# Performance work log

Measured on AMD Instinct MI355X. Metric: run time of the kernel, lower is better.

The kernel has to match this reference:

```python
import jax, jax.numpy as jnp
import numpy as np

D = 1024
K = 256
B = 8192


def setup_inputs() -> dict:
    key = jax.random.key(0)
    kx, kw, kd, kp = jax.random.split(key, 4)
    x = jax.random.normal(kx, (B, D), dtype=jnp.float32)
    # scale weights ~1/sqrt(d) so the 11-matmul chain stays numerically sane
    Ws = jax.random.normal(kw, (10, D, D), dtype=jnp.float32) / jnp.sqrt(jnp.float32(D))
    W_dec = jax.random.normal(kd, (D, K), dtype=jnp.float32) / jnp.sqrt(jnp.float32(K))
    perm = jax.random.randint(kp, (K,), 0, D, dtype=jnp.int64)
    return {"x": x, "Ws": Ws, "W_dec": W_dec, "perm": perm}


def reference(x, Ws, W_dec, perm):
    # torch nn.Linear(d,d,bias=False): y = x @ W.T
    # source applies fc1..fc9, then fc9 AGAIN, then fc10 (11 matmuls, 10 weights)
    order = list(range(9)) + [8, 9]
    h = x
    for i in order:
        h = h @ Ws[i].T  # [B, D]
    y = h[:, perm]        # vectorized gather, replaces per-row python loop [B, K]
    out = y @ W_dec.T     # fc_decode: [B, D]
    return out
```

## Files before the change

### kernel.cpp

```cpp
#include <hip/hip_runtime.h>
#include <stdint.h>
#include <stddef.h>

typedef __bf16 bf16;
typedef __bf16 bf16x8 __attribute__((ext_vector_type(8)));
typedef float f32x4 __attribute__((ext_vector_type(4)));

__device__ __forceinline__ void global_to_lds16(const void* g, void* l) {
  const __attribute__((address_space(1))) unsigned* gp =
      reinterpret_cast<const __attribute__((address_space(1))) unsigned*>(
          reinterpret_cast<uintptr_t>(g));
  __attribute__((address_space(3))) unsigned* lp =
      reinterpret_cast<__attribute__((address_space(3))) unsigned*>(
          reinterpret_cast<uintptr_t>(l));
  __builtin_amdgcn_global_load_lds(gp, lp, 16, 0, 0);
}

__device__ __forceinline__ void tile8x8_swizzle(int t, int& bx, int& by) {
  bx = (((t >> 3) & 1) << 2) | (t & 3);
  by = (((t >> 4) & 3) << 1) | ((t >> 2) & 1);
}

template <typename OutT>
__device__ __forceinline__ void gemm128_body(const bf16* __restrict__ A,
                                             const bf16* __restrict__ B,
                                             OutT* __restrict__ C,
                                             int bx, int by) {
  __shared__ bf16 As[2][128 * 64];
  __shared__ bf16 Bs[2][128 * 64];

  const int tid = threadIdx.x;
  const int wave = tid >> 6, lane = tid & 63;
  const int quad = lane >> 4, l16 = lane & 15;
  const int rowBase = by * 128;
  const int colBase = bx * 128;
  const int waveM = (wave >> 1) * 64, waveN = (wave & 1) * 64;

  const int sr = tid >> 2;
  const int sc = (tid & 3) * 8;
  const bf16* Ag0 = A + (size_t)(rowBase + sr) * 1024 + sc;
  const bf16* Ag1 = Ag0 + (size_t)64 * 1024;
  const bf16* Bg0 = B + (size_t)(colBase + sr) * 1024 + sc;
  const bf16* Bg1 = Bg0 + (size_t)64 * 1024;

  const int woff = wave * 1024;

  auto issue = [&](int k0, int p) {
    char* aB = (char*)As[p] + woff;
    char* bB = (char*)Bs[p] + woff;
    global_to_lds16(Ag0 + k0,      aB);
    global_to_lds16(Ag1 + k0,      aB + 4096);
    global_to_lds16(Ag0 + k0 + 32, aB + 8192);
    global_to_lds16(Ag1 + k0 + 32, aB + 12288);
    global_to_lds16(Bg0 + k0,      bB);
    global_to_lds16(Bg1 + k0,      bB + 4096);
    global_to_lds16(Bg0 + k0 + 32, bB + 8192);
    global_to_lds16(Bg1 + k0 + 32, bB + 12288);
  };

  f32x4 acc[4][4] = {};

  issue(0, 0);
  int p = 0;
#pragma unroll 1
  for (int k0 = 0; k0 < 1024; k0 += 64, p ^= 1) {
    __syncthreads();
    if (k0 + 64 < 1024) issue(k0 + 64, p ^ 1);
#pragma unroll
    for (int kk = 0; kk < 2; kk++) {
      const bf16* base = As[p] + kk * 4096;
      const bf16* baseB = Bs[p] + kk * 4096;
      bf16x8 af[4], bfr[4];
#pragma unroll
      for (int mi = 0; mi < 4; mi++)
        af[mi] = *(const bf16x8*)(base + (waveM + mi * 16 + l16) * 32 + quad * 8);
#pragma unroll
      for (int ni = 0; ni < 4; ni++)
        bfr[ni] = *(const bf16x8*)(baseB + (waveN + ni * 16 + l16) * 32 + quad * 8);
#pragma unroll
      for (int mi = 0; mi < 4; mi++)
#pragma unroll
        for (int ni = 0; ni < 4; ni++)
          acc[mi][ni] = __builtin_amdgcn_mfma_f32_16x16x32_bf16(af[mi], bfr[ni],
                                                                acc[mi][ni], 0, 0, 0);
    }
  }

  OutT* Cb = C + (size_t)(rowBase + waveM) * 1024 + colBase + waveN;
#pragma unroll
  for (int mi = 0; mi < 4; mi++)
#pragma unroll
    for (int ni = 0; ni < 4; ni++)
#pragma unroll
      for (int r = 0; r < 4; r++)
        Cb[(size_t)(mi * 16 + quad * 4 + r) * 1024 + ni * 16 + l16] =
            (OutT)acc[mi][ni][r];
}

struct PrepArgs {
  const float* cvt_src[5]; bf16* cvt_dst[5];
  const float* tr_src[6];  bf16* tr_dst[6];
  const float* Wdec; const int* praw; bf16* Gbf;
};

__global__ __launch_bounds__(256) void prep_all(PrepArgs p) {
  __shared__ alignas(16) char smem[64 * 65 * 2];
  const int b = blockIdx.x;
  const int tid = threadIdx.x;

  if (b < 2560) {
    const int m = b >> 9, blk = b & 511;
    const float* __restrict__ src = p.cvt_src[m];
    bf16* __restrict__ dst = p.cvt_dst[m];
    const int i = (blk * 256 + tid) * 8;
    float4 a = *(const float4*)(src + i);
    float4 c = *(const float4*)(src + i + 4);
    bf16x8 o;
    o[0] = (bf16)a.x; o[1] = (bf16)a.y; o[2] = (bf16)a.z; o[3] = (bf16)a.w;
    o[4] = (bf16)c.x; o[5] = (bf16)c.y; o[6] = (bf16)c.z; o[7] = (bf16)c.w;
    *(bf16x8*)(dst + i) = o;
  } else if (b < 4096) {
    const int t = b - 2560;
    const int m = t >> 8, r = t & 255;
    const float* __restrict__ src = p.tr_src[m];
    bf16* __restrict__ dst = p.tr_dst[m];
    bf16(*tile)[65] = reinterpret_cast<bf16(*)[65]>(smem);
    const int bx = (r & 15) * 64;
    const int by = (r >> 4) * 64;
    const int tx = tid & 63;
    const int ty4 = tid >> 6;
#pragma unroll
    for (int rr = 0; rr < 16; rr++) {
      int row = ty4 * 16 + rr;
      tile[row][tx] = (bf16)src[(size_t)(by + row) * 1024 + bx + tx];
    }
    __syncthreads();
#pragma unroll
    for (int rr = 0; rr < 16; rr++) {
      int row = ty4 * 16 + rr;
      dst[(size_t)(bx + row) * 1024 + by + tx] = tile[tx][row];
    }
  } else {
    const int j = b - 4096;
    float* row = (float*)smem;
    int* perm_l = (int*)(smem + 4096);
    int* nzp = (int*)(smem + 4096 + 1024);
#pragma unroll
    for (int c = 0; c < 4; c++) row[tid * 4 + c] = 0.f;
    if (tid == 0) *nzp = 0;
    __syncthreads();
    if (tid < 128 && p.praw[2 * tid + 1] != 0) atomicOr(nzp, 1);
    __syncthreads();
    const int is64 = (*nzp == 0);
    perm_l[tid] = is64 ? p.praw[2 * tid] : p.praw[tid];
    __syncthreads();
    atomicAdd(&row[perm_l[tid]], p.Wdec[(size_t)j * 256 + tid]);
    __syncthreads();
#pragma unroll
    for (int c = 0; c < 4; c++)
      p.Gbf[(size_t)j * 1024 + tid * 4 + c] = (bf16)row[tid * 4 + c];
  }
}

struct TreeArgs {
  const bf16* A[6]; const bf16* B[6]; bf16* C[6];
  int nG;
  const float* x; bf16* xbf; int ubase;
};

__global__ __launch_bounds__(256) void tree_level(TreeArgs a) {
  const int b = blockIdx.x;
  const int gBlocks = a.nG * 64;
  if (b < gBlocks) {
    const int z = b >> 6, t = b & 63;
    int bx, by;
    tile8x8_swizzle(t, bx, by);
    gemm128_body<bf16>(a.A[z], a.B[z], a.C[z], bx, by);
  } else {
    const int unit = a.ubase + (b - gBlocks);
    const int i = unit * 2048 + (int)threadIdx.x * 8;
    float4 v0 = *(const float4*)(a.x + i);
    float4 v1 = *(const float4*)(a.x + i + 4);
    bf16x8 o;
    o[0] = (bf16)v0.x; o[1] = (bf16)v0.y; o[2] = (bf16)v0.z; o[3] = (bf16)v0.w;
    o[4] = (bf16)v1.x; o[5] = (bf16)v1.y; o[6] = (bf16)v1.z; o[7] = (bf16)v1.w;
    *(bf16x8*)(a.xbf + i) = o;
  }
}

__global__ __launch_bounds__(256) void final_gemm(const bf16* __restrict__ A,
                                                  const bf16* __restrict__ B,
                                                  float* __restrict__ C) {
  const int b = blockIdx.x;
  gemm128_body<float>(A, B, C, b >> 6, b & 63);
}

extern "C" void kernel_launch(void* const* d_in, const int* in_sizes, int n_in,
                              void* d_out, int out_size, void* d_ws, size_t ws_size,
                              hipStream_t stream) {
  const float* x    = (const float*)d_in[0];
  const float* Wsrc = (const float*)d_in[1];
  const float* Wdec = (const float*)d_in[2];
  const int*   praw = (const int*)d_in[3];
  float* out = (float*)d_out;

  constexpr size_t MAT  = 1024ull * 1024ull;
  constexpr size_t SLOT = 2ull * 1024 * 1024;

  char* ws = (char*)d_ws;
  bf16* Wrm[5];
  for (int i = 0; i < 5; i++) Wrm[i] = (bf16*)(ws + (size_t)i * SLOT);
  bf16* Wt[6];
  for (int i = 0; i < 6; i++) Wt[i] = (bf16*)(ws + (size_t)(5 + i) * SLOT);
  bf16* Gbf = (bf16*)(ws + 11 * SLOT);
  bf16* xbf = (bf16*)(ws + 12 * SLOT);
  bf16* P[6];
  for (int i = 0; i < 6; i++) P[i] = (bf16*)(ws + (size_t)(20 + i) * SLOT);
  bf16* Q[3];
  for (int i = 0; i < 3; i++) Q[i] = (bf16*)(ws + (size_t)(26 + i) * SLOT);
  bf16* Rb = (bf16*)(ws + 29 * SLOT);
  bf16* Fb = (bf16*)(ws + 30 * SLOT);

  PrepArgs pa;
  const int rmIdx[5] = {1, 3, 5, 7, 8};
  for (int i = 0; i < 5; i++) { pa.cvt_src[i] = Wsrc + (size_t)rmIdx[i] * MAT; pa.cvt_dst[i] = Wrm[i]; }
  const int trIdx[6] = {0, 2, 4, 6, 8, 9};
  for (int i = 0; i < 6; i++) { pa.tr_src[i] = Wsrc + (size_t)trIdx[i] * MAT; pa.tr_dst[i] = Wt[i]; }
  pa.Wdec = Wdec; pa.praw = praw; pa.Gbf = Gbf;
  prep_all<<<dim3(5120), 256, 0, stream>>>(pa);

  TreeArgs L1{};
  const bf16* l1a[6] = {Gbf, Wt[4], Wrm[3], Wt[2], Wrm[1], Wt[0]};
  const bf16* l1b[6] = {Wt[5], Wrm[4], Wt[3], Wrm[2], Wt[1], Wrm[0]};
  for (int i = 0; i < 6; i++) { L1.A[i] = l1a[i]; L1.B[i] = l1b[i]; L1.C[i] = P[i]; }
  L1.nG = 6; L1.x = x; L1.xbf = xbf; L1.ubase = 0;
  tree_level<<<dim3(384), 256, 0, stream>>>(L1);

  TreeArgs L2{};
  const bf16* l2a[3] = {P[0], P[3], P[5]};
  const bf16* l2b[3] = {P[1], P[2], P[4]};
  for (int i = 0; i < 3; i++) { L2.A[i] = l2a[i]; L2.B[i] = l2b[i]; L2.C[i] = Q[i]; }
  L2.nG = 3; L2.x = x; L2.xbf = xbf; L2.ubase = 0;
  tree_level<<<dim3(192 + 1360), 256, 0, stream>>>(L2);

  TreeArgs L3{};
  L3.A[0] = Q[0]; L3.B[0] = Q[1]; L3.C[0] = Rb;
  L3.nG = 1; L3.x = x; L3.xbf = xbf; L3.ubase = 1360;
  tree_level<<<dim3(64 + 1360), 256, 0, stream>>>(L3);

  TreeArgs L4{};
  L4.A[0] = Rb; L4.B[0] = Q[2]; L4.C[0] = Fb;
  L4.nG = 1; L4.x = x; L4.xbf = xbf; L4.ubase = 2720;
  tree_level<<<dim3(64 + 1376), 256, 0, stream>>>(L4);

  final_gemm<<<dim3(512), 256, 0, stream>>>(xbf, Fb, out);

  (void)in_sizes; (void)n_in; (void)out_size; (void)ws_size;
}
```

Measured before the change: 197.1 us.

## Restructure matrix-chain tree to merge levels and overlap x-GEMM with weight products

Reassociates the weight-product tree so the activation GEMM (xbf times Q2) runs concurrently with the final weight-weight product (Q0·Q1) in one launch, removing one dependent level and kernel launch. The x-to-bf16 conversion now does eight units per block and is spread across the first two levels instead of three. This shortens the critical path of serial launches, but the final GEMM becomes S·R with both operands bf16 intermediates, which shifts where rounding happens. The changed pairing in L2 also alters the association order.

```diff
diff --git a/kernel.cpp b/kernel.cpp
--- a/kernel.cpp
+++ b/kernel.cpp
@@ -177,14 +177,34 @@
     tile8x8_swizzle(t, bx, by);
     gemm128_body<bf16>(a.A[z], a.B[z], a.C[z], bx, by);
   } else {
-    const int unit = a.ubase + (b - gBlocks);
-    const int i = unit * 2048 + (int)threadIdx.x * 8;
-    float4 v0 = *(const float4*)(a.x + i);
-    float4 v1 = *(const float4*)(a.x + i + 4);
-    bf16x8 o;
-    o[0] = (bf16)v0.x; o[1] = (bf16)v0.y; o[2] = (bf16)v0.z; o[3] = (bf16)v0.w;
-    o[4] = (bf16)v1.x; o[5] = (bf16)v1.y; o[6] = (bf16)v1.z; o[7] = (bf16)v1.w;
-    *(bf16x8*)(a.xbf + i) = o;
+    const int u0 = a.ubase + (b - gBlocks) * 8;
+#pragma unroll
+    for (int u = 0; u < 8; u++) {
+      const int i = (u0 + u) * 2048 + (int)threadIdx.x * 8;
+      float4 v0 = *(const float4*)(a.x + i);
+      float4 v1 = *(const float4*)(a.x + i + 4);
+      bf16x8 o;
+      o[0] = (bf16)v0.x; o[1] = (bf16)v0.y; o[2] = (bf16)v0.z; o[3] = (bf16)v0.w;
+      o[4] = (bf16)v1.x; o[5] = (bf16)v1.y; o[6] = (bf16)v1.z; o[7] = (bf16)v1.w;
+      *(bf16x8*)(a.xbf + i) = o;
+    }
+  }
+}
+
+struct L3SArgs {
+  const bf16* Q0; const bf16* Q1t; bf16* R;
+  const bf16* xbf; const bf16* Q2; bf16* S;
+};
+
+__global__ __launch_bounds__(256) void l3s_level(L3SArgs a) {
+  const int b = blockIdx.x;
+  if (b < 64) {
+    int bx, by;
+    tile8x8_swizzle(b, bx, by);
+    gemm128_body<bf16>(a.Q0, a.Q1t, a.R, bx, by);
+  } else {
+    const int t = b - 64;
+    gemm128_body<bf16>(a.xbf, a.Q2, a.S, t >> 6, t & 63);
   }
 }
 
@@ -219,7 +239,7 @@
   bf16* Q[3];
   for (int i = 0; i < 3; i++) Q[i] = (bf16*)(ws + (size_t)(26 + i) * SLOT);
   bf16* Rb = (bf16*)(ws + 29 * SLOT);
-  bf16* Fb = (bf16*)(ws + 30 * SLOT);
+  bf16* Sb = (bf16*)(ws + 31 * SLOT);
 
   PrepArgs pa;
   const int rmIdx[5] = {1, 3, 5, 7, 8};
@@ -234,26 +254,21 @@
   const bf16* l1b[6] = {Wt[5], Wrm[4], Wt[3], Wrm[2], Wt[1], Wrm[0]};
   for (int i = 0; i < 6; i++) { L1.A[i] = l1a[i]; L1.B[i] = l1b[i]; L1.C[i] = P[i]; }
   L1.nG = 6; L1.x = x; L1.xbf = xbf; L1.ubase = 0;
-  tree_level<<<dim3(384), 256, 0, stream>>>(L1);
+  tree_level<<<dim3(384 + 256), 256, 0, stream>>>(L1);
 
   TreeArgs L2{};
-  const bf16* l2a[3] = {P[0], P[3], P[5]};
-  const bf16* l2b[3] = {P[1], P[2], P[4]};
+  const bf16* l2a[3] = {P[0], P[3], P[4]};
+  const bf16* l2b[3] = {P[1], P[2], P[5]};
   for (int i = 0; i < 3; i++) { L2.A[i] = l2a[i]; L2.B[i] = l2b[i]; L2.C[i] = Q[i]; }
-  L2.nG = 3; L2.x = x; L2.xbf = xbf; L2.ubase = 0;
-  tree_level<<<dim3(192 + 1360), 256, 0, stream>>>(L2);
-
-  TreeArgs L3{};
-  L3.A[0] = Q[0]; L3.B[0] = Q[1]; L3.C[0] = Rb;
-  L3.nG = 1; L3.x = x; L3.xbf = xbf; L3.ubase = 1360;
-  tree_level<<<dim3(64 + 1360), 256, 0, stream>>>(L3);
-
-  TreeArgs L4{};
-  L4.A[0] = Rb; L4.B[0] = Q[2]; L4.C[0] = Fb;
-  L4.nG = 1; L4.x = x; L4.xbf = xbf; L4.ubase = 2720;
-  tree_level<<<dim3(64 + 1376), 256, 0, stream>>>(L4);
-
-  final_gemm<<<dim3(512), 256, 0, stream>>>(xbf, Fb, out);
+  L2.nG = 3; L2.x = x; L2.xbf = xbf; L2.ubase = 2048;
+  tree_level<<<dim3(192 + 256), 256, 0, stream>>>(L2);
+
+  L3SArgs l3;
+  l3.Q0 = Q[0]; l3.Q1t = Q[1]; l3.R = Rb;
+  l3.xbf = xbf; l3.Q2 = Q[2]; l3.S = Sb;
+  l3s_level<<<dim3(576), 256, 0, stream>>>(l3);
+
+  final_gemm<<<dim3(512), 256, 0, stream>>>(Sb, Rb, out);
 
   (void)in_sizes; (void)n_in; (void)out_size; (void)ws_size;
 }
```

Measured after the change: 201.7 us. 1.02x slower.

## Deepen GEMM LDS pipeline to four K=32 stages and rebalance x conversion blocks

Applied to the files above, without the earlier changes.

The 128x128 GEMM main loop now uses four K=32 LDS stages with three tiles in flight. It replaces __syncthreads with explicit vmcnt waits and a raw barrier, so global-to-LDS loads overlap more MFMA work. The x fp32-to-bf16 conversion blocks each handle eight units and are spread across levels 1 and 2 only, which shrinks the extra grids attached to levels 2 to 4. The manual waitcnt logic depends on exact instruction counts and adds race risk. It also changes how the conversion traffic overlaps with the GEMMs.

```diff
diff --git a/kernel.cpp b/kernel.cpp
--- a/kernel.cpp
+++ b/kernel.cpp
@@ -26,8 +26,8 @@
                                              const bf16* __restrict__ B,
                                              OutT* __restrict__ C,
                                              int bx, int by) {
-  __shared__ bf16 As[2][128 * 64];
-  __shared__ bf16 Bs[2][128 * 64];
+  __shared__ bf16 As[4][128 * 32];
+  __shared__ bf16 Bs[4][128 * 32];
 
   const int tid = threadIdx.x;
   const int wave = tid >> 6, lane = tid & 63;
@@ -45,45 +45,43 @@
 
   const int woff = wave * 1024;
 
-  auto issue = [&](int k0, int p) {
-    char* aB = (char*)As[p] + woff;
-    char* bB = (char*)Bs[p] + woff;
-    global_to_lds16(Ag0 + k0,      aB);
-    global_to_lds16(Ag1 + k0,      aB + 4096);
-    global_to_lds16(Ag0 + k0 + 32, aB + 8192);
-    global_to_lds16(Ag1 + k0 + 32, aB + 12288);
-    global_to_lds16(Bg0 + k0,      bB);
-    global_to_lds16(Bg1 + k0,      bB + 4096);
-    global_to_lds16(Bg0 + k0 + 32, bB + 8192);
-    global_to_lds16(Bg1 + k0 + 32, bB + 12288);
+  auto issue = [&](int k0, int c) {
+    char* aB = (char*)As[c] + woff;
+    char* bB = (char*)Bs[c] + woff;
+    global_to_lds16(Ag0 + k0, aB);
+    global_to_lds16(Ag1 + k0, aB + 4096);
+    global_to_lds16(Bg0 + k0, bB);
+    global_to_lds16(Bg1 + k0, bB + 4096);
   };
 
   f32x4 acc[4][4] = {};
 
-  issue(0, 0);
-  int p = 0;
+  issue(0, 0); issue(32, 1); issue(64, 2);
+
 #pragma unroll 1
-  for (int k0 = 0; k0 < 1024; k0 += 64, p ^= 1) {
-    __syncthreads();
-    if (k0 + 64 < 1024) issue(k0 + 64, p ^ 1);
-#pragma unroll
-    for (int kk = 0; kk < 2; kk++) {
-      const bf16* base = As[p] + kk * 4096;
-      const bf16* baseB = Bs[p] + kk * 4096;
-      bf16x8 af[4], bfr[4];
-#pragma unroll
-      for (int mi = 0; mi < 4; mi++)
-        af[mi] = *(const bf16x8*)(base + (waveM + mi * 16 + l16) * 32 + quad * 8);
+  for (int i = 0; i < 32; ++i) {
+    if (i < 30)       asm volatile("s_waitcnt vmcnt(8)" ::: "memory");
+    else if (i == 30) asm volatile("s_waitcnt vmcnt(4)" ::: "memory");
+    else              asm volatile("s_waitcnt vmcnt(0)" ::: "memory");
+    __builtin_amdgcn_s_barrier();
+    __builtin_amdgcn_sched_barrier(0);
+    if (i < 29) issue((i + 3) * 32, (i + 3) & 3);
+
+    const bf16* base  = As[i & 3];
+    const bf16* baseB = Bs[i & 3];
+    bf16x8 af[4], bfr[4];
+#pragma unroll
+    for (int mi = 0; mi < 4; mi++)
+      af[mi] = *(const bf16x8*)(base + (waveM + mi * 16 + l16) * 32 + quad * 8);
+#pragma unroll
+    for (int ni = 0; ni < 4; ni++)
+      bfr[ni] = *(const bf16x8*)(baseB + (waveN + ni * 16 + l16) * 32 + quad * 8);
+#pragma unroll
+    for (int mi = 0; mi < 4; mi++)
 #pragma unroll
       for (int ni = 0; ni < 4; ni++)
-        bfr[ni] = *(const bf16x8*)(baseB + (waveN + ni * 16 + l16) * 32 + quad * 8);
-#pragma unroll
-      for (int mi = 0; mi < 4; mi++)
-#pragma unroll
-        for (int ni = 0; ni < 4; ni++)
-          acc[mi][ni] = __builtin_amdgcn_mfma_f32_16x16x32_bf16(af[mi], bfr[ni],
-                                                                acc[mi][ni], 0, 0, 0);
-    }
+        acc[mi][ni] = __builtin_amdgcn_mfma_f32_16x16x32_bf16(af[mi], bfr[ni],
+                                                              acc[mi][ni], 0, 0, 0);
   }
 
   OutT* Cb = C + (size_t)(rowBase + waveM) * 1024 + colBase + waveN;
@@ -177,14 +175,17 @@
     tile8x8_swizzle(t, bx, by);
     gemm128_body<bf16>(a.A[z], a.B[z], a.C[z], bx, by);
   } else {
-    const int unit = a.ubase + (b - gBlocks);
-    const int i = unit * 2048 + (int)threadIdx.x * 8;
-    float4 v0 = *(const float4*)(a.x + i);
-    float4 v1 = *(const float4*)(a.x + i + 4);
-    bf16x8 o;
-    o[0] = (bf16)v0.x; o[1] = (bf16)v0.y; o[2] = (bf16)v0.z; o[3] = (bf16)v0.w;
-    o[4] = (bf16)v1.x; o[5] = (bf16)v1.y; o[6] = (bf16)v1.z; o[7] = (bf16)v1.w;
-    *(bf16x8*)(a.xbf + i) = o;
+    const int u0 = a.ubase + (b - gBlocks) * 8;
+#pragma unroll
+    for (int u = 0; u < 8; u++) {
+      const int i = (u0 + u) * 2048 + (int)threadIdx.x * 8;
+      float4 v0 = *(const float4*)(a.x + i);
+      float4 v1 = *(const float4*)(a.x + i + 4);
+      bf16x8 o;
+      o[0] = (bf16)v0.x; o[1] = (bf16)v0.y; o[2] = (bf16)v0.z; o[3] = (bf16)v0.w;
+      o[4] = (bf16)v1.x; o[5] = (bf16)v1.y; o[6] = (bf16)v1.z; o[7] = (bf16)v1.w;
+      *(bf16x8*)(a.xbf + i) = o;
+    }
   }
 }
 
@@ -234,24 +235,24 @@
   const bf16* l1b[6] = {Wt[5], Wrm[4], Wt[3], Wrm[2], Wt[1], Wrm[0]};
   for (int i = 0; i < 6; i++) { L1.A[i] = l1a[i]; L1.B[i] = l1b[i]; L1.C[i] = P[i]; }
   L1.nG = 6; L1.x = x; L1.xbf = xbf; L1.ubase = 0;
-  tree_level<<<dim3(384), 256, 0, stream>>>(L1);
+  tree_level<<<dim3(384 + 256), 256, 0, stream>>>(L1);
 
   TreeArgs L2{};
   const bf16* l2a[3] = {P[0], P[3], P[5]};
   const bf16* l2b[3] = {P[1], P[2], P[4]};
   for (int i = 0; i < 3; i++) { L2.A[i] = l2a[i]; L2.B[i] = l2b[i]; L2.C[i] = Q[i]; }
-  L2.nG = 3; L2.x = x; L2.xbf = xbf; L2.ubase = 0;
-  tree_level<<<dim3(192 + 1360), 256, 0, stream>>>(L2);
+  L2.nG = 3; L2.x = x; L2.xbf = xbf; L2.ubase = 2048;
+  tree_level<<<dim3(192 + 256), 256, 0, stream>>>(L2);
 
   TreeArgs L3{};
   L3.A[0] = Q[0]; L3.B[0] = Q[1]; L3.C[0] = Rb;
-  L3.nG = 1; L3.x = x; L3.xbf = xbf; L3.ubase = 1360;
-  tree_level<<<dim3(64 + 1360), 256, 0, stream>>>(L3);
+  L3.nG = 1; L3.x = x; L3.xbf = xbf; L3.ubase = 4096;
+  tree_level<<<dim3(64), 256, 0, stream>>>(L3);
 
   TreeArgs L4{};
   L4.A[0] = Rb; L4.B[0] = Q[2]; L4.C[0] = Fb;
-  L4.nG = 1; L4.x = x; L4.xbf = xbf; L4.ubase = 2720;
-  tree_level<<<dim3(64 + 1376), 256, 0, stream>>>(L4);
+  L4.nG = 1; L4.x = x; L4.xbf = xbf; L4.ubase = 4096;
+  tree_level<<<dim3(64), 256, 0, stream>>>(L4);
 
   final_gemm<<<dim3(512), 256, 0, stream>>>(xbf, Fb, out);
 
```

Result: slower. 209.6 us (+6.4%).

## Switch GEMMs to 256x128 tiles with 512 threads and XOR-swizzled LDS

Applied to the files above, without the earlier changes.

Replaces the 128x128 GEMM body with a 256x128 tile run by 8 waves. Staging now loads full 64-wide K rows with an XOR swizzle on the 16-byte chunk index, so fragment reads avoid LDS bank conflicts. The fp32-to-bf16 conversion of x moves into the first two tree levels, with 16 units per block, and the last two levels become pure GEMMs. The larger tile raises data reuse per block, but it halves the block count: the single-GEMM levels get only 32 blocks, and each block holds 96KB of LDS, which limits occupancy.

```diff
diff --git a/kernel.cpp b/kernel.cpp
--- a/kernel.cpp
+++ b/kernel.cpp
@@ -4,6 +4,7 @@
 
 typedef __bf16 bf16;
 typedef __bf16 bf16x8 __attribute__((ext_vector_type(8)));
+typedef __bf16 bf16x4 __attribute__((ext_vector_type(4)));
 typedef float f32x4 __attribute__((ext_vector_type(4)));
 
 __device__ __forceinline__ void global_to_lds16(const void* g, void* l) {
@@ -16,67 +17,63 @@
   __builtin_amdgcn_global_load_lds(gp, lp, 16, 0, 0);
 }
 
-__device__ __forceinline__ void tile8x8_swizzle(int t, int& bx, int& by) {
-  bx = (((t >> 3) & 1) << 2) | (t & 3);
-  by = (((t >> 4) & 3) << 1) | ((t >> 2) & 1);
-}
-
 template <typename OutT>
-__device__ __forceinline__ void gemm128_body(const bf16* __restrict__ A,
-                                             const bf16* __restrict__ B,
-                                             OutT* __restrict__ C,
-                                             int bx, int by) {
-  __shared__ bf16 As[2][128 * 64];
+__device__ __forceinline__ void gemm256x128_body(const bf16* __restrict__ A,
+                                                 const bf16* __restrict__ B,
+                                                 OutT* __restrict__ C,
+                                                 int bx, int by) {
+  __shared__ bf16 As[2][256 * 64];
   __shared__ bf16 Bs[2][128 * 64];
 
   const int tid = threadIdx.x;
   const int wave = tid >> 6, lane = tid & 63;
   const int quad = lane >> 4, l16 = lane & 15;
-  const int rowBase = by * 128;
+  const int rowBase = by * 256;
   const int colBase = bx * 128;
-  const int waveM = (wave >> 1) * 64, waveN = (wave & 1) * 64;
-
-  const int sr = tid >> 2;
-  const int sc = (tid & 3) * 8;
-  const bf16* Ag0 = A + (size_t)(rowBase + sr) * 1024 + sc;
-  const bf16* Ag1 = Ag0 + (size_t)64 * 1024;
-  const bf16* Bg0 = B + (size_t)(colBase + sr) * 1024 + sc;
-  const bf16* Bg1 = Bg0 + (size_t)64 * 1024;
-
-  const int woff = wave * 1024;
+  const int waveM = (wave >> 1) * 64;
+  const int waveN = (wave & 1) * 64;
+
+  const int srow = tid >> 3;
+  const int scol = (((tid & 7) ^ ((tid >> 3) & 7)) << 3);
+  const bf16* Ag = A + (size_t)(rowBase + srow) * 1024 + scol;
+  const bf16* Bg = B + (size_t)(colBase + srow) * 1024 + scol;
+  const int ldsoff = wave * 1024;
 
   auto issue = [&](int k0, int p) {
-    char* aB = (char*)As[p] + woff;
-    char* bB = (char*)Bs[p] + woff;
-    global_to_lds16(Ag0 + k0,      aB);
-    global_to_lds16(Ag1 + k0,      aB + 4096);
-    global_to_lds16(Ag0 + k0 + 32, aB + 8192);
-    global_to_lds16(Ag1 + k0 + 32, aB + 12288);
-    global_to_lds16(Bg0 + k0,      bB);
-    global_to_lds16(Bg1 + k0,      bB + 4096);
-    global_to_lds16(Bg0 + k0 + 32, bB + 8192);
-    global_to_lds16(Bg1 + k0 + 32, bB + 12288);
+    char* aB = (char*)As[p] + ldsoff;
+    char* bB = (char*)Bs[p] + ldsoff;
+#pragma unroll
+    for (int c = 0; c < 4; c++)
+      global_to_lds16(Ag + k0 + (size_t)c * 64 * 1024, aB + c * 8192);
+#pragma unroll
+    for (int c = 0; c < 2; c++)
+      global_to_lds16(Bg + k0 + (size_t)c * 64 * 1024, bB + c * 8192);
   };
 
   f32x4 acc[4][4] = {};
 
   issue(0, 0);
   int p = 0;
+  const int swz = l16 & 7;
 #pragma unroll 1
   for (int k0 = 0; k0 < 1024; k0 += 64, p ^= 1) {
     __syncthreads();
     if (k0 + 64 < 1024) issue(k0 + 64, p ^ 1);
 #pragma unroll
     for (int kk = 0; kk < 2; kk++) {
-      const bf16* base = As[p] + kk * 4096;
-      const bf16* baseB = Bs[p] + kk * 4096;
       bf16x8 af[4], bfr[4];
 #pragma unroll
-      for (int mi = 0; mi < 4; mi++)
-        af[mi] = *(const bf16x8*)(base + (waveM + mi * 16 + l16) * 32 + quad * 8);
-#pragma unroll
-      for (int ni = 0; ni < 4; ni++)
-        bfr[ni] = *(const bf16x8*)(baseB + (waveN + ni * 16 + l16) * 32 + quad * 8);
+      for (int mi = 0; mi < 4; mi++) {
+        const int row = waveM + mi * 16 + l16;
+        const int g = ((kk << 2) + quad) ^ swz;
+        af[mi] = *(const bf16x8*)(As[p] + row * 64 + g * 8);
+      }
+#pragma unroll
+      for (int ni = 0; ni < 4; ni++) {
+        const int row = waveN + ni * 16 + l16;
+        const int g = ((kk << 2) + quad) ^ swz;
+        bfr[ni] = *(const bf16x8*)(Bs[p] + row * 64 + g * 8);
+      }
 #pragma unroll
       for (int mi = 0; mi < 4; mi++)
 #pragma unroll
@@ -168,31 +165,33 @@
   const float* x; bf16* xbf; int ubase;
 };
 
-__global__ __launch_bounds__(256) void tree_level(TreeArgs a) {
+__global__ __launch_bounds__(512) void tree_level(TreeArgs a) {
   const int b = blockIdx.x;
-  const int gBlocks = a.nG * 64;
+  const int gBlocks = a.nG * 32;
   if (b < gBlocks) {
-    const int z = b >> 6, t = b & 63;
-    int bx, by;
-    tile8x8_swizzle(t, bx, by);
-    gemm128_body<bf16>(a.A[z], a.B[z], a.C[z], bx, by);
+    const int z = b >> 5, t = b & 31;
+    gemm256x128_body<bf16>(a.A[z], a.B[z], a.C[z], t >> 2, t & 3);
   } else {
-    const int unit = a.ubase + (b - gBlocks);
-    const int i = unit * 2048 + (int)threadIdx.x * 8;
-    float4 v0 = *(const float4*)(a.x + i);
-    float4 v1 = *(const float4*)(a.x + i + 4);
-    bf16x8 o;
-    o[0] = (bf16)v0.x; o[1] = (bf16)v0.y; o[2] = (bf16)v0.z; o[3] = (bf16)v0.w;
-    o[4] = (bf16)v1.x; o[5] = (bf16)v1.y; o[6] = (bf16)v1.z; o[7] = (bf16)v1.w;
-    *(bf16x8*)(a.xbf + i) = o;
+    const int u0 = a.ubase + (b - gBlocks) * 16;
+#pragma unroll
+    for (int u = 0; u < 16; u++) {
+      const int i = (u0 + u) * 2048 + (int)threadIdx.x * 4;
+      float4 v = *(const float4*)(a.x + i);
+      bf16x4 o;
+      o[0] = (bf16)v.x; o[1] = (bf16)v.y; o[2] = (bf16)v.z; o[3] = (bf16)v.w;
+      *(bf16x4*)(a.xbf + i) = o;
+    }
   }
 }
 
-__global__ __launch_bounds__(256) void final_gemm(const bf16* __restrict__ A,
+__global__ __launch_bounds__(512) void final_gemm(const bf16* __restrict__ A,
                                                   const bf16* __restrict__ B,
                                                   float* __restrict__ C) {
   const int b = blockIdx.x;
-  gemm128_body<float>(A, B, C, b >> 6, b & 63);
+  const int j = b >> 3;
+  const int by = (b & 7) * 4 + (j & 3);
+  const int bx = j >> 2;
+  gemm256x128_body<float>(A, B, C, bx, by);
 }
 
 extern "C" void kernel_launch(void* const* d_in, const int* in_sizes, int n_in,
@@ -234,26 +233,26 @@
   const bf16* l1b[6] = {Wt[5], Wrm[4], Wt[3], Wrm[2], Wt[1], Wrm[0]};
   for (int i = 0; i < 6; i++) { L1.A[i] = l1a[i]; L1.B[i] = l1b[i]; L1.C[i] = P[i]; }
   L1.nG = 6; L1.x = x; L1.xbf = xbf; L1.ubase = 0;
-  tree_level<<<dim3(384), 256, 0, stream>>>(L1);
+  tree_level<<<dim3(192 + 128), 512, 0, stream>>>(L1);
 
   TreeArgs L2{};
   const bf16* l2a[3] = {P[0], P[3], P[5]};
   const bf16* l2b[3] = {P[1], P[2], P[4]};
   for (int i = 0; i < 3; i++) { L2.A[i] = l2a[i]; L2.B[i] = l2b[i]; L2.C[i] = Q[i]; }
-  L2.nG = 3; L2.x = x; L2.xbf = xbf; L2.ubase = 0;
-  tree_level<<<dim3(192 + 1360), 256, 0, stream>>>(L2);
+  L2.nG = 3; L2.x = x; L2.xbf = xbf; L2.ubase = 2048;
+  tree_level<<<dim3(96 + 128), 512, 0, stream>>>(L2);
 
   TreeArgs L3{};
   L3.A[0] = Q[0]; L3.B[0] = Q[1]; L3.C[0] = Rb;
-  L3.nG = 1; L3.x = x; L3.xbf = xbf; L3.ubase = 1360;
-  tree_level<<<dim3(64 + 1360), 256, 0, stream>>>(L3);
+  L3.nG = 1; L3.x = x; L3.xbf = xbf; L3.ubase = 4096;
+  tree_level<<<dim3(32), 512, 0, stream>>>(L3);
 
   TreeArgs L4{};
   L4.A[0] = Rb; L4.B[0] = Q[2]; L4.C[0] = Fb;
-  L4.nG = 1; L4.x = x; L4.xbf = xbf; L4.ubase = 2720;
-  tree_level<<<dim3(64 + 1376), 256, 0, stream>>>(L4);
-
-  final_gemm<<<dim3(512), 256, 0, stream>>>(xbf, Fb, out);
+  L4.nG = 1; L4.x = x; L4.xbf = xbf; L4.ubase = 4096;
+  tree_level<<<dim3(32), 512, 0, stream>>>(L4);
+
+  final_gemm<<<dim3(256), 512, 0, stream>>>(xbf, Fb, out);
 
   (void)in_sizes; (void)n_in; (void)out_size; (void)ws_size;
 }
```

Measured after the change: 210.4 us. +6.7%, slower.
